# Kernel tuning notes

Hardware: AMD Instinct MI355X
Metric: run time of the kernel (lower is better)

Reference implementation:

```python
import jax, jax.numpy as jnp
import numpy as np

B, C, H, W = 16, 256, 64, 64
HID, N, SD, NH, HD, NC = 256, 300, 64, 4, 16, 80


def _conv1x1(x, w, b):
    # x: (B,Cin,H,W), w: (Cout,Cin)
    return jnp.einsum('bchw,oc->bohw', x, w) + b[None, :, None, None]


def _lin(x, w, b):
    return x @ w.T + b


def _ln(x, g, b, eps=1e-5):
    mu = x.mean(-1, keepdims=True)
    var = ((x - mu) ** 2).mean(-1, keepdims=True)
    return (x - mu) / jnp.sqrt(var + eps) * g + b


def setup_inputs() -> dict:
    key = jax.random.key(0)
    ks = jax.random.split(key, 16)
    def w(k, shape, s=0.02):
        return jax.random.normal(k, shape, jnp.float32) * s
    return {
        'x': jax.random.normal(ks[0], (B, C, H, W), jnp.float32),
        'spotlight_sources': w(ks[1], (N, SD)),
        'pos_w': w(ks[2], (HID // 2, 2)), 'pos_b': jnp.zeros((HID // 2,), jnp.float32),
        'fp_w': w(ks[3], (HID, C)), 'fp_b': jnp.zeros((HID,), jnp.float32),
        'bn_g': jnp.ones((HID,), jnp.float32), 'bn_b': jnp.zeros((HID,), jnp.float32),
        'bn_m': jnp.zeros((HID,), jnp.float32), 'bn_v': jnp.ones((HID,), jnp.float32),
        'key_w': w(ks[4], (SD, HID)), 'key_b': jnp.zeros((SD,), jnp.float32),
        'val_w': w(ks[5], (HID, HID)), 'val_b': jnp.zeros((HID,), jnp.float32),
        'ctp_w': w(ks[6], (NC, HID)), 'ctp_b': jnp.zeros((NC,), jnp.float32),
        'bb1_w': w(ks[7], (HID, HID)), 'bb1_b': jnp.zeros((HID,), jnp.float32),
        'bbln_g': jnp.ones((HID,), jnp.float32), 'bbln_b': jnp.zeros((HID,), jnp.float32),
        'bb2_w': w(ks[8], (HID // 2, HID)), 'bb2_b': jnp.zeros((HID // 2,), jnp.float32),
        'bb3_w': w(ks[9], (4, HID // 2)), 'bb3_b': jnp.zeros((4,), jnp.float32),
        'ch1_w': w(ks[10], (HID, HID)), 'ch1_b': jnp.zeros((HID,), jnp.float32),
        'chln_g': jnp.ones((HID,), jnp.float32), 'chln_b': jnp.zeros((HID,), jnp.float32),
        'ch2_w': w(ks[11], (HID // 2, HID)), 'ch2_b': jnp.zeros((HID // 2,), jnp.float32),
        'ch3_w': w(ks[12], (1, HID // 2)), 'ch3_b': jnp.zeros((1,), jnp.float32),
    }


def _forward(x, spotlight_sources, pos_w, pos_b, fp_w, fp_b, bn_g, bn_b, bn_m, bn_v,
             key_w, key_b, val_w, val_b, ctp_w, ctp_b,
             bb1_w, bb1_b, bbln_g, bbln_b, bb2_w, bb2_b, bb3_w, bb3_b,
             ch1_w, ch1_b, chln_g, chln_b, ch2_w, ch2_b, ch3_w, ch3_b):
    Bv, _, Hh, Ww = x.shape
    # position encoding: 2-channel normalized (y, x) grid, conv1x1 to HID//2
    y = jnp.linspace(-1.0, 1.0, Hh, dtype=jnp.float32)
    xc = jnp.linspace(-1.0, 1.0, Ww, dtype=jnp.float32)
    coords = jnp.stack([jnp.broadcast_to(y[:, None], (Hh, Ww)),
                        jnp.broadcast_to(xc[None, :], (Hh, Ww))], 0)[None]  # (1,2,H,W)
    # feature_proj: conv1x1 + BatchNorm(eval) + ReLU
    feats = _conv1x1(x, fp_w, fp_b)
    feats = (feats - bn_m[None, :, None, None]) / jnp.sqrt(bn_v[None, :, None, None] + 1e-5)
    feats = jax.nn.relu(feats * bn_g[None, :, None, None] + bn_b[None, :, None, None])
    pos = jnp.broadcast_to(_conv1x1(coords, pos_w, pos_b), (Bv, HID // 2, Hh, Ww))
    comb = jnp.concatenate([feats[:, :HID // 2], pos], axis=1)  # (B,HID,H,W)
    keys = _conv1x1(comb, key_w, key_b).reshape(Bv, NH, HD, Hh * Ww)   # (B,h,d,M)
    vals = _conv1x1(comb, val_w, val_b).reshape(Bv, HID, Hh * Ww)      # (B,HID,M)
    q = spotlight_sources.reshape(N, NH, HD)                            # (N,h,d)
    logits = jnp.einsum('nhd,bhdm->bhnm', q, keys) / jnp.sqrt(jnp.float32(HD))
    attn = jax.nn.softmax(logits, axis=-1).mean(axis=1)                 # (B,N,M), head-averaged
    maps = attn.reshape(Bv, N, Hh, Ww)
    sf = jnp.einsum('bnm,bcm->bnc', attn, vals)                         # (B,N,HID)
    def head(z, w1, b1, g, bb, w2, b2, w3, b3):
        z = jax.nn.relu(_ln(_lin(z, w1, b1), g, bb))
        z = jax.nn.relu(_lin(z, w2, b2))
        return _lin(z, w3, b3)
    boxes = head(sf, bb1_w, bb1_b, bbln_g, bbln_b, bb2_w, bb2_b, bb3_w, bb3_b)
    scores = jax.nn.sigmoid(head(sf, ch1_w, ch1_b, chln_g, chln_b, ch2_w, ch2_b, ch3_w, ch3_b))
    cls = _lin(sf, ctp_w, ctp_b)
    # diversity loss: mean off-diagonal cosine similarity of attention rows
    an = attn / jnp.maximum(jnp.linalg.norm(attn, axis=2, keepdims=True), 1e-12)
    sim = jnp.einsum('bnm,bkm->bnk', an, an)
    div = (sim.sum() - jnp.einsum('bnn->', sim)) / (N * (N - 1)) * 0.1
    return boxes, scores, cls, maps, div, sf


def reference(x, spotlight_sources, pos_w, pos_b, fp_w, fp_b, bn_g, bn_b, bn_m, bn_v,
              key_w, key_b, val_w, val_b, ctp_w, ctp_b,
              bb1_w, bb1_b, bbln_g, bbln_b, bb2_w, bb2_b, bb3_w, bb3_b,
              ch1_w, ch1_b, chln_g, chln_b, ch2_w, ch2_b, ch3_w, ch3_b):
    return _forward(x, spotlight_sources, pos_w, pos_b, fp_w, fp_b, bn_g, bn_b, bn_m, bn_v,
                    key_w, key_b, val_w, val_b, ctp_w, ctp_b,
                    bb1_w, bb1_b, bbln_g, bbln_b, bb2_w, bb2_b, bb3_w, bb3_b,
                    ch1_w, ch1_b, chln_g, chln_b, ch2_w, ch2_b, ch3_w, ch3_b)
```

## Files before the change

kernel.cpp:

```cpp
#include <hip/hip_runtime.h>
#include <math.h>

#define BB 16
#define CIN 256
#define MM 4096
#define HIDC 256
#define NQ 300
#define NHH 4
#define HDD 16

#define OFF_BOXES  0
#define OFF_SCORES 19200
#define OFF_CLS    24000
#define OFF_MAPS   408000
#define OFF_DIV    20068800
#define OFF_SF     20068801

#define WS_COMB16  0
#define WS_KEYS16  8388608
#define WS_ATTN16  10485760
#define WS_T32     20316160
#define WS_T16     21544960
#define WS_VALW16  22159360
#define WS_SUMS    22192128
#define WS_NORM    22211328
#define WS_ACC     22216128
#define WS_P       22216192

#define HP_SF16   (WS_P + 0)
#define HP_Z1PRE  (WS_P + 614400)
#define HP_Z1_16  (WS_P + 1843200)
#define HP_Z2BB   (WS_P + 2457600)
#define HP_Z2CH   (WS_P + 2764800)
#define HP_HW     (WS_P + 3072000)
#define WS_Q16    (WS_P + 3200000)
#define WS_XT     25426432
#define WS_COMBT  33815040
#define WS_FPW16  42203648
#define WS_KEYW16 42220032

#define HW_BB1 0
#define HW_CH1 65536
#define HW_BB2 131072
#define HW_CH2 163840
#define HW_CTP 196608

typedef short short8 __attribute__((ext_vector_type(8)));
typedef float floatx4 __attribute__((ext_vector_type(4)));

__device__ __forceinline__ unsigned short f2bf(float f){
  unsigned int u = __float_as_uint(f);
  u = (u + 0x7FFFu + ((u >> 16) & 1u)) >> 16;
  return (unsigned short)u;
}
__device__ __forceinline__ float bf1(unsigned short u){
  return __uint_as_float((unsigned int)u << 16);
}

__global__ void zero_kernel(float* p){ p[0] = 0.f; }

__global__ __launch_bounds__(256) void zero4_kernel(float4* __restrict__ p, int n4){
  int i = blockIdx.x * 256 + threadIdx.x;
  if (i < n4) p[i] = make_float4(0.f, 0.f, 0.f, 0.f);
}

__global__ __launch_bounds__(256) void cast_sum4_kernel(const float* __restrict__ part,
                                                        unsigned short* __restrict__ dst, int n4){
  int i = blockIdx.x * 256 + threadIdx.x;
  if (i < n4){
    int b = i / 19200, r = i - b * 19200;
    const float4* p0 = (const float4*)part + (size_t)(b*4 + 0) * 19200 + r;
    const float4* p1 = (const float4*)part + (size_t)(b*4 + 1) * 19200 + r;
    const float4* p2 = (const float4*)part + (size_t)(b*4 + 2) * 19200 + r;
    const float4* p3 = (const float4*)part + (size_t)(b*4 + 3) * 19200 + r;
    float4 a = *p0, bq = *p1, c = *p2, d = *p3;
    float4 v;
    v.x = a.x + bq.x + c.x + d.x;
    v.y = a.y + bq.y + c.y + d.y;
    v.z = a.z + bq.z + c.z + d.z;
    v.w = a.w + bq.w + c.w + d.w;
    ushort4 u;
    u.x = f2bf(v.x); u.y = f2bf(v.y); u.z = f2bf(v.z); u.w = f2bf(v.w);
    ((ushort4*)dst)[i] = u;
  }
}

__global__ __launch_bounds__(256) void castq_kernel(const float* __restrict__ ss,
                                                    unsigned short* __restrict__ q16){
  int i = blockIdx.x * 256 + threadIdx.x;
  if (i < 320*64)
    q16[i] = (i < NQ*64) ? f2bf(ss[i] * 0.25f) : (unsigned short)0;
}

__global__ __launch_bounds__(256) void cast_w2_kernel(const float* __restrict__ fp_w,
    const float* __restrict__ key_w,
    unsigned short* __restrict__ fpw16, unsigned short* __restrict__ keyw16){
  int i = blockIdx.x * 256 + threadIdx.x;
  if (i < 128*256) fpw16[i] = f2bf(fp_w[i]);
  if (i < 64*256)  keyw16[i] = f2bf(key_w[i]);
}

__global__ __launch_bounds__(256) void cast_heads_kernel(
    const float* __restrict__ val_w, const float* __restrict__ bb1_w,
    const float* __restrict__ ch1_w, const float* __restrict__ bb2_w,
    const float* __restrict__ ch2_w, const float* __restrict__ ctp_w,
    unsigned short* __restrict__ valw16, unsigned short* __restrict__ hw16){
  int i = blockIdx.x * 256 + threadIdx.x;
  int T = gridDim.x * 256;
  for (int j = i; j < 65536; j += T) valw16[j] = f2bf(val_w[j]);
  for (int j = i; j < 65536; j += T) hw16[HW_BB1 + j] = f2bf(bb1_w[j]);
  for (int j = i; j < 65536; j += T) hw16[HW_CH1 + j] = f2bf(ch1_w[j]);
  for (int j = i; j < 32768; j += T) hw16[HW_BB2 + j] = f2bf(bb2_w[j]);
  for (int j = i; j < 32768; j += T) hw16[HW_CH2 + j] = f2bf(ch2_w[j]);
  for (int j = i; j < 20480; j += T) hw16[HW_CTP + j] = f2bf(ctp_w[j]);
}

__global__ __launch_bounds__(256) void pos_fill_kernel(const float* __restrict__ pos_w,
                                                       const float* __restrict__ pos_b,
                                                       unsigned short* __restrict__ comb16){
  int lin = blockIdx.x * 256 + threadIdx.x;
  int m  = (lin & 1023) * 4;
  int c  = (lin >> 10) & 127;
  int b  = lin >> 17;
  int row = m >> 6, col = m & 63;
  float y  = -1.f + 2.f * (float)row / 63.f;
  float wy = pos_w[c*2], wx = pos_w[c*2+1], pb = pos_b[c];
  float base = wy * y + pb;
  ushort4 u;
  u.x = f2bf(base + wx * (-1.f + 2.f * (float)(col+0) / 63.f));
  u.y = f2bf(base + wx * (-1.f + 2.f * (float)(col+1) / 63.f));
  u.z = f2bf(base + wx * (-1.f + 2.f * (float)(col+2) / 63.f));
  u.w = f2bf(base + wx * (-1.f + 2.f * (float)(col+3) / 63.f));
  *(ushort4*)&comb16[((size_t)(b*HIDC + 128 + c))*MM + m] = u;
}

__global__ __launch_bounds__(256) void pos_fillT_kernel(const float* __restrict__ pos_w,
                                                        const float* __restrict__ pos_b,
                                                        unsigned short* __restrict__ combT){
  int lin = blockIdx.x * 256 + threadIdx.x;
  int c4 = (lin & 31) * 4;
  int m  = lin >> 5;
  int row = m >> 6, col = m & 63;
  float y = -1.f + 2.f * (float)row / 63.f;
  float x = -1.f + 2.f * (float)col / 63.f;
  ushort4 u;
  u.x = f2bf(pos_w[(c4+0)*2] * y + pos_w[(c4+0)*2+1] * x + pos_b[c4+0]);
  u.y = f2bf(pos_w[(c4+1)*2] * y + pos_w[(c4+1)*2+1] * x + pos_b[c4+1]);
  u.z = f2bf(pos_w[(c4+2)*2] * y + pos_w[(c4+2)*2+1] * x + pos_b[c4+2]);
  u.w = f2bf(pos_w[(c4+3)*2] * y + pos_w[(c4+3)*2+1] * x + pos_b[c4+3]);
  #pragma unroll
  for (int b = 0; b < BB; b++)
    *(ushort4*)&combT[((size_t)b*MM + m)*CIN + 128 + c4] = u;
}

template<bool INF32>
__global__ __launch_bounds__(256) void transpose_kernel(
    const void* __restrict__ in, unsigned short* __restrict__ outp){
  int b = blockIdx.z;
  int m0 = blockIdx.x * 64;
  int r0 = blockIdx.y * 64;
  __shared__ unsigned short lds[64][68];
  int t = threadIdx.x;
  if (INF32){
    const float* ib = (const float*)in + (size_t)b * CIN * MM;
    #pragma unroll
    for (int j = 0; j < 4; j++){
      int lin = j*256 + t;
      int rr = lin >> 4;
      int m4 = (lin & 15) * 4;
      float4 v = *(const float4*)&ib[(size_t)(r0 + rr)*MM + m0 + m4];
      lds[m4+0][rr] = f2bf(v.x);
      lds[m4+1][rr] = f2bf(v.y);
      lds[m4+2][rr] = f2bf(v.z);
      lds[m4+3][rr] = f2bf(v.w);
    }
  } else {
    const unsigned short* ib = (const unsigned short*)in + (size_t)b * CIN * MM;
    #pragma unroll
    for (int j = 0; j < 4; j++){
      int lin = j*256 + t;
      int rr = lin >> 4;
      int m4 = (lin & 15) * 4;
      ushort4 v = *(const ushort4*)&ib[(size_t)(r0 + rr)*MM + m0 + m4];
      lds[m4+0][rr] = v.x; lds[m4+1][rr] = v.y;
      lds[m4+2][rr] = v.z; lds[m4+3][rr] = v.w;
    }
  }
  __syncthreads();
  unsigned short* ob = outp + (size_t)b * MM * CIN;
  #pragma unroll
  for (int j = 0; j < 4; j++){
    int lin = j*256 + t;
    int mm = lin >> 4;
    int c4 = (lin & 15) * 4;
    ushort4 u;
    u.x = lds[mm][c4+0]; u.y = lds[mm][c4+1];
    u.z = lds[mm][c4+2]; u.w = lds[mm][c4+3];
    *(ushort4*)&ob[(size_t)(m0 + mm)*CIN + r0 + c4] = u;
  }
}

__global__ __launch_bounds__(64) void comb_mfma_kernel(
    const unsigned short* __restrict__ fpw16, const unsigned short* __restrict__ xT16,
    const float* __restrict__ fp_b, const float* __restrict__ bn_g,
    const float* __restrict__ bn_b, const float* __restrict__ bn_m,
    const float* __restrict__ bn_v, unsigned short* __restrict__ comb16){
  int b = blockIdx.z;
  const unsigned short* Bb = xT16 + (size_t)b * MM * CIN;
  unsigned short* cb = comb16 + (size_t)b * HIDC * MM;
  int lane = threadIdx.x;
  int r16 = lane & 15;
  int ko  = (lane >> 4) * 8;
  const unsigned short* arow[4];
  const unsigned short* brow[4];
  #pragma unroll
  for (int i = 0; i < 4; i++){
    arow[i] = fpw16 + (size_t)(blockIdx.y*64 + i*16 + r16) * CIN + ko;
    brow[i] = Bb + (size_t)(blockIdx.x*64 + i*16 + r16) * CIN + ko;
  }
  floatx4 acc[4][4];
  #pragma unroll
  for (int i = 0; i < 4; i++)
    #pragma unroll
    for (int j = 0; j < 4; j++)
      acc[i][j] = (floatx4){0.f, 0.f, 0.f, 0.f};
  short8 a[4], bv[4], a2[4], b2[4];
  #pragma unroll
  for (int i = 0; i < 4; i++){
    a[i]  = *(const short8*)(arow[i]);
    bv[i] = *(const short8*)(brow[i]);
  }
  for (int k = 32; k < CIN; k += 32){
    #pragma unroll
    for (int i = 0; i < 4; i++){
      a2[i] = *(const short8*)(arow[i] + k);
      b2[i] = *(const short8*)(brow[i] + k);
    }
    #pragma unroll
    for (int i = 0; i < 4; i++)
      #pragma unroll
      for (int j = 0; j < 4; j++)
        acc[i][j] = __builtin_amdgcn_mfma_f32_16x16x32_bf16(a[i], bv[j], acc[i][j], 0, 0, 0);
    #pragma unroll
    for (int i = 0; i < 4; i++){ a[i] = a2[i]; bv[i] = b2[i]; }
  }
  #pragma unroll
  for (int i = 0; i < 4; i++)
    #pragma unroll
    for (int j = 0; j < 4; j++)
      acc[i][j] = __builtin_amdgcn_mfma_f32_16x16x32_bf16(a[i], bv[j], acc[i][j], 0, 0, 0);
  int cq = lane & 15, rq = (lane >> 4) * 4;
  #pragma unroll
  for (int i = 0; i < 4; i++){
    #pragma unroll
    for (int reg = 0; reg < 4; reg++){
      int rr = blockIdx.y*64 + i*16 + rq + reg;
      float sc  = rsqrtf(bn_v[rr] + 1e-5f);
      float mul = sc * bn_g[rr];
      float ofs = (fp_b[rr] - bn_m[rr]) * mul + bn_b[rr];
      #pragma unroll
      for (int j = 0; j < 4; j++){
        int cc = blockIdx.x*64 + j*16 + cq;
        float v = fmaxf(acc[i][j][reg] * mul + ofs, 0.f);
        cb[(size_t)rr * MM + cc] = f2bf(v);
      }
    }
  }
}


__global__ __launch_bounds__(256) void attn_sums_kernel(
    const unsigned short* __restrict__ q16, const unsigned short* __restrict__ keysT,
    float* __restrict__ sums){
  int b = blockIdx.z, ny = blockIdx.y, mx = blockIdx.x;
  int tid = threadIdx.x, w = tid >> 6, lane = tid & 63;
  int n0 = ny * 64;
  int l15 = lane & 15, qh = lane >> 4;
  int ko = (qh & 1) * 8;
  bool lo = lane < 32;
  const unsigned short* kT = keysT + (size_t)b * MM * 64;
  int mwb = mx*128 + w*32;
  __shared__ unsigned short qlds[64][72];
  __shared__ float spart[4][NHH][64];
  for (int c = tid; c < 512; c += 256){
    int r = c >> 3, d8 = (c & 7) * 8;
    *(short8*)&qlds[r][d8] = *(const short8*)&q16[(size_t)(n0 + r)*64 + d8];
  }
  __syncthreads();
  short8 zz = {0,0,0,0,0,0,0,0};
  #pragma unroll 1
  for (int h = 0; h < NHH; h++){
    short8 bq[4];
    #pragma unroll
    for (int ni = 0; ni < 4; ni++)
      bq[ni] = lo ? *(const short8*)&qlds[ni*16 + l15][h*16 + ko] : zz;
    float sacc[4] = {0.f, 0.f, 0.f, 0.f};
    #pragma unroll
    for (int ms = 0; ms < 2; ms++){
      int m = mwb + ms*16 + l15;
      short8 a = lo ? *(const short8*)&kT[(size_t)m*64 + h*16 + ko] : zz;
      #pragma unroll
      for (int ni = 0; ni < 4; ni++){
        floatx4 l = __builtin_amdgcn_mfma_f32_16x16x32_bf16(a, bq[ni],
                        (floatx4){0.f,0.f,0.f,0.f}, 0, 0, 0);
        sacc[ni] += __expf(l[0]) + __expf(l[1]) + __expf(l[2]) + __expf(l[3]);
      }
    }
    #pragma unroll
    for (int ni = 0; ni < 4; ni++){
      float v = sacc[ni];
      v += __shfl_xor(v, 16); v += __shfl_xor(v, 32);
      if (lane < 16) spart[w][h][ni*16 + lane] = v;
    }
  }
  __syncthreads();
  if (tid < NHH*64){
    int h = tid >> 6, r = tid & 63, n = n0 + r;
    if (n < NQ){
      float v = spart[0][h][r] + spart[1][h][r] + spart[2][h][r] + spart[3][h][r];
      atomicAdd(&sums[((size_t)b*NHH + h)*NQ + n], v);
    }
  }
}

__global__ __launch_bounds__(256) void attn_emit_kernel(
    const unsigned short* __restrict__ q16, const unsigned short* __restrict__ keysT,
    const float* __restrict__ sums, float* __restrict__ maps,
    unsigned short* __restrict__ attn16, float* __restrict__ norms){
  int b = blockIdx.z, ny = blockIdx.y, mx = blockIdx.x;
  int tid = threadIdx.x, w = tid >> 6, lane = tid & 63;
  int n0 = ny * 64;
  int l15 = lane & 15, qh = lane >> 4;
  int ko = (qh & 1) * 8;
  bool lo = lane < 32;
  __shared__ unsigned short qlds[64][72];
  __shared__ float inv_s[NHH][64];
  __shared__ float npart[4][64];
  for (int c = tid; c < 512; c += 256){
    int r = c >> 3, d8 = (c & 7) * 8;
    *(short8*)&qlds[r][d8] = *(const short8*)&q16[(size_t)(n0 + r)*64 + d8];
  }
  if (tid < NHH*64){
    int h = tid >> 6, r = tid & 63, n = n0 + r;
    inv_s[h][r] = (n < NQ) ? 0.25f / sums[((size_t)b*NHH + h)*NQ + n] : 0.f;
  }
  __syncthreads();
  const unsigned short* kT = keysT + (size_t)b * MM * 64;
  int mwb = mx*128 + w*32;
  short8 zz = {0,0,0,0,0,0,0,0};
  float nacc[4] = {0.f, 0.f, 0.f, 0.f};
  float* mb = maps + (size_t)b * NQ * MM;
  unsigned short* ab = attn16 + (size_t)b * NQ * MM;
  #pragma unroll 1
  for (int ms = 0; ms < 2; ms++){
    asm volatile("" ::: "memory");
    int mbase = mwb + ms*16;
    int mk = mbase + l15;
    floatx4 o[4];
    #pragma unroll
    for (int ni = 0; ni < 4; ni++) o[ni] = (floatx4){0.f,0.f,0.f,0.f};
    #pragma unroll
    for (int h = 0; h < NHH; h++){
      short8 a = lo ? *(const short8*)&kT[(size_t)mk*64 + h*16 + ko] : zz;
      #pragma unroll
      for (int ni = 0; ni < 4; ni++){
        short8 bq = lo ? *(const short8*)&qlds[ni*16 + l15][h*16 + ko] : zz;
        floatx4 l = __builtin_amdgcn_mfma_f32_16x16x32_bf16(a, bq,
                        (floatx4){0.f,0.f,0.f,0.f}, 0, 0, 0);
        float iv = inv_s[h][ni*16 + l15];
        o[ni][0] += __expf(l[0]) * iv;
        o[ni][1] += __expf(l[1]) * iv;
        o[ni][2] += __expf(l[2]) * iv;
        o[ni][3] += __expf(l[3]) * iv;
      }
    }
    #pragma unroll
    for (int ni = 0; ni < 4; ni++){
      nacc[ni] += o[ni][0]*o[ni][0] + o[ni][1]*o[ni][1]
                + o[ni][2]*o[ni][2] + o[ni][3]*o[ni][3];
      int n = n0 + ni*16 + l15;
      if (n < NQ){
        size_t off = (size_t)n*MM + mbase + qh*4;
        float4 v; v.x = o[ni][0]; v.y = o[ni][1]; v.z = o[ni][2]; v.w = o[ni][3];
        *(float4*)&mb[off] = v;
        ushort4 u;
        u.x = f2bf(v.x); u.y = f2bf(v.y); u.z = f2bf(v.z); u.w = f2bf(v.w);
        *(ushort4*)&ab[off] = u;
      }
    }
  }
  #pragma unroll
  for (int ni = 0; ni < 4; ni++){
    float v = nacc[ni];
    v += __shfl_xor(v, 16); v += __shfl_xor(v, 32);
    if (lane < 16) npart[w][ni*16 + lane] = v;
  }
  __syncthreads();
  if (tid < 64){
    int n = n0 + tid;
    if (n < NQ){
      float v = npart[0][tid] + npart[1][tid] + npart[2][tid] + npart[3][tid];
      atomicAdd(&norms[(size_t)b*NQ + n], v);
    }
  }
}

template<bool RELU>
__global__ __launch_bounds__(64) void mfma_nt_kernel(
    const unsigned short* __restrict__ A, size_t sA,
    const unsigned short* __restrict__ B, size_t sB,
    const float* __restrict__ bias,
    float* __restrict__ C, unsigned short* __restrict__ C16,
    size_t sC, int ldc, int Mr, int Nc, int K){
  int bz = blockIdx.z;
  const unsigned short* Ab = A + (size_t)bz * sA;
  const unsigned short* Bb = B + (size_t)bz * sB;
  int lane = threadIdx.x;
  int r16 = lane & 15;
  int ko  = (lane >> 4) * 8;
  const unsigned short* arow[4];
  const unsigned short* brow[4];
  #pragma unroll
  for (int i = 0; i < 4; i++){
    int m = blockIdx.y*64 + i*16 + r16;
    if (m > Mr - 1) m = Mr - 1;
    arow[i] = Ab + (size_t)m * K + ko;
    int n = blockIdx.x*64 + i*16 + r16;
    if (n > Nc - 1) n = Nc - 1;
    brow[i] = Bb + (size_t)n * K + ko;
  }
  floatx4 acc[4][4];
  #pragma unroll
  for (int i = 0; i < 4; i++)
    #pragma unroll
    for (int j = 0; j < 4; j++)
      acc[i][j] = (floatx4){0.f, 0.f, 0.f, 0.f};
  short8 a[4], bv[4], a2[4], b2[4];
  #pragma unroll
  for (int i = 0; i < 4; i++){
    a[i]  = *(const short8*)(arow[i]);
    bv[i] = *(const short8*)(brow[i]);
  }
  for (int k = 32; k < K; k += 32){
    #pragma unroll
    for (int i = 0; i < 4; i++){
      a2[i] = *(const short8*)(arow[i] + k);
      b2[i] = *(const short8*)(brow[i] + k);
    }
    #pragma unroll
    for (int i = 0; i < 4; i++)
      #pragma unroll
      for (int j = 0; j < 4; j++)
        acc[i][j] = __builtin_amdgcn_mfma_f32_16x16x32_bf16(a[i], bv[j], acc[i][j], 0, 0, 0);
    #pragma unroll
    for (int i = 0; i < 4; i++){ a[i] = a2[i]; bv[i] = b2[i]; }
  }
  #pragma unroll
  for (int i = 0; i < 4; i++)
    #pragma unroll
    for (int j = 0; j < 4; j++)
      acc[i][j] = __builtin_amdgcn_mfma_f32_16x16x32_bf16(a[i], bv[j], acc[i][j], 0, 0, 0);
  int cq = lane & 15, rq = (lane >> 4) * 4;
  #pragma unroll
  for (int j = 0; j < 4; j++){
    int cc = blockIdx.x*64 + j*16 + cq;
    if (cc >= Nc) continue;
    float bv_ = bias ? bias[cc] : 0.f;
    #pragma unroll
    for (int i = 0; i < 4; i++){
      int rbase = blockIdx.y*64 + i*16 + rq;
      #pragma unroll
      for (int reg = 0; reg < 4; reg++){
        int rr = rbase + reg;
        if (rr < Mr){
          float v = acc[i][j][reg] + bv_;
          if (RELU) v = fmaxf(v, 0.f);
          size_t o = (size_t)bz * sC + (size_t)rr * ldc + cc;
          if (C)   C[o] = v;
          if (C16) C16[o] = f2bf(v);
        }
      }
    }
  }
}

__global__ __launch_bounds__(64) void mfma_nt_splitk_kernel(
    const unsigned short* __restrict__ A, size_t sA,
    const unsigned short* __restrict__ B, size_t sB,
    float* __restrict__ C, size_t sC, int ldc, int Mr, int K, int kchunk){
  int nks = K / kchunk;
  int bz = blockIdx.z / nks;
  int kz = blockIdx.z % nks;
  const unsigned short* Ab = A + (size_t)bz * sA + (size_t)kz * kchunk;
  const unsigned short* Bb = B + (size_t)bz * sB + (size_t)kz * kchunk;
  int lane = threadIdx.x;
  int r16 = lane & 15;
  int ko  = (lane >> 4) * 8;
  const unsigned short* arow[4];
  const unsigned short* brow[4];
  #pragma unroll
  for (int i = 0; i < 4; i++){
    int m = blockIdx.y*64 + i*16 + r16;
    if (m > Mr - 1) m = Mr - 1;
    arow[i] = Ab + (size_t)m * K + ko;
    int n = blockIdx.x*64 + i*16 + r16;
    brow[i] = Bb + (size_t)n * K + ko;
  }
  floatx4 acc[4][4];
  #pragma unroll
  for (int i = 0; i < 4; i++)
    #pragma unroll
    for (int j = 0; j < 4; j++)
      acc[i][j] = (floatx4){0.f, 0.f, 0.f, 0.f};
  short8 a[4], bv[4], a2[4], b2[4];
  #pragma unroll
  for (int i = 0; i < 4; i++){
    a[i]  = *(const short8*)(arow[i]);
    bv[i] = *(const short8*)(brow[i]);
  }
  for (int k = 32; k < kchunk; k += 32){
    #pragma unroll
    for (int i = 0; i < 4; i++){
      a2[i] = *(const short8*)(arow[i] + k);
      b2[i] = *(const short8*)(brow[i] + k);
    }
    #pragma unroll
    for (int i = 0; i < 4; i++)
      #pragma unroll
      for (int j = 0; j < 4; j++)
        acc[i][j] = __builtin_amdgcn_mfma_f32_16x16x32_bf16(a[i], bv[j], acc[i][j], 0, 0, 0);
    #pragma unroll
    for (int i = 0; i < 4; i++){ a[i] = a2[i]; bv[i] = b2[i]; }
  }
  #pragma unroll
  for (int i = 0; i < 4; i++)
    #pragma unroll
    for (int j = 0; j < 4; j++)
      acc[i][j] = __builtin_amdgcn_mfma_f32_16x16x32_bf16(a[i], bv[j], acc[i][j], 0, 0, 0);
  int cq = lane & 15, rq = (lane >> 4) * 4;
  #pragma unroll
  for (int j = 0; j < 4; j++){
    int cc = blockIdx.x*64 + j*16 + cq;
    #pragma unroll
    for (int i = 0; i < 4; i++){
      int rbase = blockIdx.y*64 + i*16 + rq;
      #pragma unroll
      for (int reg = 0; reg < 4; reg++){
        int rr = rbase + reg;
        if (rr < Mr)
          C[(size_t)blockIdx.z * sC + (size_t)rr * ldc + cc] = acc[i][j][reg];
      }
    }
  }
}

__global__ __launch_bounds__(256) void ln_relu_kernel(const float* __restrict__ zin,
    const float* __restrict__ g, const float* __restrict__ bvec,
    unsigned short* __restrict__ zout){
  int row = blockIdx.x * 4 + (threadIdx.x >> 6);
  int lane = threadIdx.x & 63;
  float4 v = *(const float4*)&zin[(size_t)row * 256 + lane * 4];
  float s = v.x + v.y + v.z + v.w;
  #pragma unroll
  for (int off = 32; off >= 1; off >>= 1) s += __shfl_xor(s, off);
  float mean = s * (1.f/256.f);
  float dx = v.x - mean, dy = v.y - mean, dz = v.z - mean, dw = v.w - mean;
  float sq = dx*dx + dy*dy + dz*dz + dw*dw;
  #pragma unroll
  for (int off = 32; off >= 1; off >>= 1) sq += __shfl_xor(sq, off);
  float inv = rsqrtf(sq * (1.f/256.f) + 1e-5f);
  float4 gv = *(const float4*)&g[lane * 4];
  float4 bb = *(const float4*)&bvec[lane * 4];
  ushort4 u;
  u.x = f2bf(fmaxf(dx*inv*gv.x + bb.x, 0.f));
  u.y = f2bf(fmaxf(dy*inv*gv.y + bb.y, 0.f));
  u.z = f2bf(fmaxf(dz*inv*gv.z + bb.z, 0.f));
  u.w = f2bf(fmaxf(dw*inv*gv.w + bb.w, 0.f));
  *(ushort4*)&zout[(size_t)row * 256 + lane * 4] = u;
}

__global__ __launch_bounds__(256) void head3_kernel(
    const unsigned short* __restrict__ z2bb, const unsigned short* __restrict__ z2ch,
    const float* __restrict__ bb3_w, const float* __restrict__ bb3_b,
    const float* __restrict__ ch3_w, const float* __restrict__ ch3_b,
    float* __restrict__ boxes, float* __restrict__ scores){
  int row = blockIdx.x * 4 + (threadIdx.x >> 6);
  int lane = threadIdx.x & 63;
  float zb0 = bf1(z2bb[(size_t)row*128 + 2*lane]);
  float zb1 = bf1(z2bb[(size_t)row*128 + 2*lane + 1]);
  float zc0 = bf1(z2ch[(size_t)row*128 + 2*lane]);
  float zc1 = bf1(z2ch[(size_t)row*128 + 2*lane + 1]);
  float acc[5];
  #pragma unroll
  for (int o = 0; o < 4; o++)
    acc[o] = bb3_w[o*128 + 2*lane]*zb0 + bb3_w[o*128 + 2*lane + 1]*zb1;
  acc[4] = ch3_w[2*lane]*zc0 + ch3_w[2*lane + 1]*zc1;
  #pragma unroll
  for (int o = 0; o < 5; o++){
    float v = acc[o];
    #pragma unroll
    for (int off = 32; off >= 1; off >>= 1) v += __shfl_xor(v, off);
    acc[o] = v;
  }
  if (lane == 0){
    #pragma unroll
    for (int o = 0; o < 4; o++)
      boxes[(size_t)row*4 + o] = acc[o] + bb3_b[o];
    float sv = acc[4] + ch3_b[0];
    scores[row] = 1.f / (1.f + __expf(-sv));
  }
}

__global__ __launch_bounds__(256) void simdiv_kernel(const unsigned short* __restrict__ attn16,
    const float* __restrict__ norms, float* __restrict__ acc){
  int b = blockIdx.y;
  int m = blockIdx.x * 256 + threadIdx.x;
  __shared__ float inv_s[NQ];
  __shared__ float red[4];
  for (int i = threadIdx.x; i < NQ; i += 256)
    inv_s[i] = 1.f / fmaxf(sqrtf(norms[(size_t)b * NQ + i]), 1e-12f);
  __syncthreads();
  const unsigned short* ab = attn16 + (size_t)b * NQ * MM;
  float S = 0.f;
  for (int n = 0; n < NQ; n++)
    S += bf1(ab[(size_t)n * MM + m]) * inv_s[n];
  float p = S * S;
  #pragma unroll
  for (int off = 32; off >= 1; off >>= 1) p += __shfl_xor(p, off);
  int w = threadIdx.x >> 6, lane = threadIdx.x & 63;
  if (lane == 0) red[w] = p;
  __syncthreads();
  if (threadIdx.x == 0) atomicAdd(acc, red[0] + red[1] + red[2] + red[3]);
}

__global__ void finalize_kernel(const float* __restrict__ acc, float* __restrict__ out_div){
  out_div[0] = (acc[0] - (float)(BB * NQ)) / (float)(NQ * (NQ - 1)) * 0.1f;
}

extern "C" void kernel_launch(void* const* d_in, const int* in_sizes, int n_in,
                              void* d_out, int out_size, void* d_ws, size_t ws_size,
                              hipStream_t stream){
  const float* x      = (const float*)d_in[0];
  const float* ss     = (const float*)d_in[1];
  const float* pos_w  = (const float*)d_in[2];
  const float* pos_b  = (const float*)d_in[3];
  const float* fp_w   = (const float*)d_in[4];
  const float* fp_b   = (const float*)d_in[5];
  const float* bn_g   = (const float*)d_in[6];
  const float* bn_b   = (const float*)d_in[7];
  const float* bn_m   = (const float*)d_in[8];
  const float* bn_v   = (const float*)d_in[9];
  const float* key_w  = (const float*)d_in[10];
  const float* key_b  = (const float*)d_in[11];
  const float* val_w  = (const float*)d_in[12];
  const float* val_b  = (const float*)d_in[13];
  const float* ctp_w  = (const float*)d_in[14];
  const float* ctp_b  = (const float*)d_in[15];
  const float* bb1_w  = (const float*)d_in[16];
  const float* bb1_b  = (const float*)d_in[17];
  const float* bbln_g = (const float*)d_in[18];
  const float* bbln_b = (const float*)d_in[19];
  const float* bb2_w  = (const float*)d_in[20];
  const float* bb2_b  = (const float*)d_in[21];
  const float* bb3_w  = (const float*)d_in[22];
  const float* bb3_b  = (const float*)d_in[23];
  const float* ch1_w  = (const float*)d_in[24];
  const float* ch1_b  = (const float*)d_in[25];
  const float* chln_g = (const float*)d_in[26];
  const float* chln_b = (const float*)d_in[27];
  const float* ch2_w  = (const float*)d_in[28];
  const float* ch2_b  = (const float*)d_in[29];
  const float* ch3_w  = (const float*)d_in[30];
  const float* ch3_b  = (const float*)d_in[31];

  float* out    = (float*)d_out;
  float* boxes  = out + OFF_BOXES;
  float* scores = out + OFF_SCORES;
  float* cls    = out + OFF_CLS;
  float* maps   = out + OFF_MAPS;
  float* divp   = out + OFF_DIV;
  float* sfout  = out + OFF_SF;

  float* ws = (float*)d_ws;
  unsigned short* comb16 = (unsigned short*)(ws + WS_COMB16);
  unsigned short* keysT  = (unsigned short*)(ws + WS_KEYS16);
  unsigned short* attn16 = (unsigned short*)(ws + WS_ATTN16);
  unsigned short* t16    = (unsigned short*)(ws + WS_T16);
  unsigned short* valw16 = (unsigned short*)(ws + WS_VALW16);
  float* sums  = ws + WS_SUMS;
  float* norms = ws + WS_NORM;
  float* dacc  = ws + WS_ACC;
  unsigned short* sf16   = (unsigned short*)(ws + HP_SF16);
  float*          z1pre  = ws + HP_Z1PRE;
  unsigned short* z1_16  = (unsigned short*)(ws + HP_Z1_16);
  unsigned short* z2bb16 = (unsigned short*)(ws + HP_Z2BB);
  unsigned short* z2ch16 = (unsigned short*)(ws + HP_Z2CH);
  unsigned short* hw16   = (unsigned short*)(ws + HP_HW);
  unsigned short* q16    = (unsigned short*)(ws + WS_Q16);
  unsigned short* xT16   = (unsigned short*)(ws + WS_XT);
  float*          tpart  = ws + WS_XT;
  unsigned short* combT  = (unsigned short*)(ws + WS_COMBT);
  unsigned short* fpw16  = (unsigned short*)(ws + WS_FPW16);
  unsigned short* keyw16 = (unsigned short*)(ws + WS_KEYW16);

  zero_kernel<<<1, 1, 0, stream>>>(dacc);
  zero4_kernel<<<24, 256, 0, stream>>>((float4*)sums, 6000);
  castq_kernel<<<80, 256, 0, stream>>>(ss, q16);
  cast_w2_kernel<<<128, 256, 0, stream>>>(fp_w, key_w, fpw16, keyw16);

  transpose_kernel<true><<<dim3(64,4,16), 256, 0, stream>>>(x, xT16);
  pos_fill_kernel<<<8192, 256, 0, stream>>>(pos_w, pos_b, comb16);
  pos_fillT_kernel<<<512, 256, 0, stream>>>(pos_w, pos_b, combT);
  comb_mfma_kernel<<<dim3(64,2,16), 64, 0, stream>>>(
      fpw16, xT16, fp_b, bn_g, bn_b, bn_m, bn_v, comb16);
  transpose_kernel<false><<<dim3(64,2,16), 256, 0, stream>>>(comb16, combT);
  mfma_nt_kernel<false><<<dim3(1,64,16), 64, 0, stream>>>(
      combT, (size_t)MM*CIN, keyw16, 0, key_b,
      nullptr, keysT, (size_t)MM*64, 64, MM, 64, CIN);

  attn_sums_kernel<<<dim3(32,5,16), 256, 0, stream>>>(q16, keysT, sums);
  attn_emit_kernel<<<dim3(32,5,16), 256, 0, stream>>>(q16, keysT, sums, maps, attn16, norms);

  mfma_nt_splitk_kernel<<<dim3(4,5,BB*4), 64, 0, stream>>>(
      attn16, (size_t)NQ*MM, comb16, (size_t)HIDC*MM,
      tpart, (size_t)NQ*HIDC, HIDC, NQ, MM, MM/4);
  cast_sum4_kernel<<<1200, 256, 0, stream>>>(tpart, t16, 307200);
  cast_heads_kernel<<<256, 256, 0, stream>>>(val_w, bb1_w, ch1_w, bb2_w, ch2_w, ctp_w, valw16, hw16);
  mfma_nt_kernel<false><<<dim3(4,5,BB), 64, 0, stream>>>(
      t16, (size_t)NQ*HIDC, valw16, 0, val_b,
      sfout, sf16, (size_t)NQ*HIDC, HIDC, NQ, HIDC, HIDC);

  mfma_nt_kernel<false><<<dim3(4,75,1), 64, 0, stream>>>(
      sf16, 0, hw16 + HW_BB1, 0, bb1_b, z1pre, nullptr, 0, 256, 4800, 256, 256);
  ln_relu_kernel<<<1200, 256, 0, stream>>>(z1pre, bbln_g, bbln_b, z1_16);
  mfma_nt_kernel<true><<<dim3(2,75,1), 64, 0, stream>>>(
      z1_16, 0, hw16 + HW_BB2, 0, bb2_b, nullptr, z2bb16, 0, 128, 4800, 128, 256);
  mfma_nt_kernel<false><<<dim3(4,75,1), 64, 0, stream>>>(
      sf16, 0, hw16 + HW_CH1, 0, ch1_b, z1pre, nullptr, 0, 256, 4800, 256, 256);
  ln_relu_kernel<<<1200, 256, 0, stream>>>(z1pre, chln_g, chln_b, z1_16);
  mfma_nt_kernel<true><<<dim3(2,75,1), 64, 0, stream>>>(
      z1_16, 0, hw16 + HW_CH2, 0, ch2_b, nullptr, z2ch16, 0, 128, 4800, 128, 256);
  head3_kernel<<<1200, 256, 0, stream>>>(z2bb16, z2ch16, bb3_w, bb3_b, ch3_w, ch3_b, boxes, scores);
  mfma_nt_kernel<false><<<dim3(2,75,1), 64, 0, stream>>>(
      sf16, 0, hw16 + HW_CTP, 0, ctp_b, cls, nullptr, 0, 80, 4800, 80, 256);

  simdiv_kernel<<<dim3(16,16), 256, 0, stream>>>(attn16, norms, dacc);
  finalize_kernel<<<1, 1, 0, stream>>>(dacc, divp);
}
```

Measured before the change: 514.1 us.

## Fuse small kernels, batch head GEMMs, in-block split-K reduce, drop comb transpose

Merges several setup cast kernels and the two positional-fill kernels into single launches. The comb conv epilogue now writes the transposed layout directly, so the separate bf16 transpose pass is removed. The split-K attention-value GEMM now reduces its four K-slices in shared memory within one 256-thread block and emits bf16, removing the fp32 partial buffer and the cast_sum pass. The box and score head GEMMs and their LayerNorms are batched over z with a per-batch bias stride. Together these reduce launch count and global memory traffic, at the cost of scattered 8-byte transposed stores and a four-phase serialized LDS reduction.

```diff
diff --git a/kernel.cpp b/kernel.cpp
--- a/kernel.cpp
+++ b/kernel.cpp
@@ -19,7 +19,6 @@
 #define WS_COMB16  0
 #define WS_KEYS16  8388608
 #define WS_ATTN16  10485760
-#define WS_T32     20316160
 #define WS_T16     21544960
 #define WS_VALW16  22159360
 #define WS_SUMS    22192128
@@ -28,16 +27,17 @@
 #define WS_P       22216192
 
 #define HP_SF16   (WS_P + 0)
-#define HP_Z1PRE  (WS_P + 614400)
-#define HP_Z1_16  (WS_P + 1843200)
 #define HP_Z2BB   (WS_P + 2457600)
 #define HP_Z2CH   (WS_P + 2764800)
 #define HP_HW     (WS_P + 3072000)
+#define WS_B2     (WS_P + 3180544)
 #define WS_Q16    (WS_P + 3200000)
 #define WS_XT     25426432
 #define WS_COMBT  33815040
 #define WS_FPW16  42203648
 #define WS_KEYW16 42220032
+#define WS_Z1PRE2 42228224
+#define WS_Z1B16  44685824
 
 #define HW_BB1 0
 #define HW_CH1 65536
@@ -57,54 +57,30 @@
   return __uint_as_float((unsigned int)u << 16);
 }
 
-__global__ void zero_kernel(float* p){ p[0] = 0.f; }
-
 __global__ __launch_bounds__(256) void zero4_kernel(float4* __restrict__ p, int n4){
   int i = blockIdx.x * 256 + threadIdx.x;
   if (i < n4) p[i] = make_float4(0.f, 0.f, 0.f, 0.f);
 }
 
-__global__ __launch_bounds__(256) void cast_sum4_kernel(const float* __restrict__ part,
-                                                        unsigned short* __restrict__ dst, int n4){
+__global__ __launch_bounds__(256) void init_kernel(const float* __restrict__ ss,
+    const float* __restrict__ fp_w, const float* __restrict__ key_w,
+    unsigned short* __restrict__ q16, unsigned short* __restrict__ fpw16,
+    unsigned short* __restrict__ keyw16){
   int i = blockIdx.x * 256 + threadIdx.x;
-  if (i < n4){
-    int b = i / 19200, r = i - b * 19200;
-    const float4* p0 = (const float4*)part + (size_t)(b*4 + 0) * 19200 + r;
-    const float4* p1 = (const float4*)part + (size_t)(b*4 + 1) * 19200 + r;
-    const float4* p2 = (const float4*)part + (size_t)(b*4 + 2) * 19200 + r;
-    const float4* p3 = (const float4*)part + (size_t)(b*4 + 3) * 19200 + r;
-    float4 a = *p0, bq = *p1, c = *p2, d = *p3;
-    float4 v;
-    v.x = a.x + bq.x + c.x + d.x;
-    v.y = a.y + bq.y + c.y + d.y;
-    v.z = a.z + bq.z + c.z + d.z;
-    v.w = a.w + bq.w + c.w + d.w;
-    ushort4 u;
-    u.x = f2bf(v.x); u.y = f2bf(v.y); u.z = f2bf(v.z); u.w = f2bf(v.w);
-    ((ushort4*)dst)[i] = u;
-  }
-}
-
-__global__ __launch_bounds__(256) void castq_kernel(const float* __restrict__ ss,
-                                                    unsigned short* __restrict__ q16){
-  int i = blockIdx.x * 256 + threadIdx.x;
-  if (i < 320*64)
-    q16[i] = (i < NQ*64) ? f2bf(ss[i] * 0.25f) : (unsigned short)0;
-}
-
-__global__ __launch_bounds__(256) void cast_w2_kernel(const float* __restrict__ fp_w,
-    const float* __restrict__ key_w,
-    unsigned short* __restrict__ fpw16, unsigned short* __restrict__ keyw16){
-  int i = blockIdx.x * 256 + threadIdx.x;
-  if (i < 128*256) fpw16[i] = f2bf(fp_w[i]);
-  if (i < 64*256)  keyw16[i] = f2bf(key_w[i]);
+  int T = gridDim.x * 256;
+  for (int j = i; j < 320*64; j += T)
+    q16[j] = (j < NQ*64) ? f2bf(ss[j] * 0.25f) : (unsigned short)0;
+  for (int j = i; j < 128*256; j += T) fpw16[j] = f2bf(fp_w[j]);
+  for (int j = i; j < 64*256; j += T)  keyw16[j] = f2bf(key_w[j]);
 }
 
 __global__ __launch_bounds__(256) void cast_heads_kernel(
     const float* __restrict__ val_w, const float* __restrict__ bb1_w,
     const float* __restrict__ ch1_w, const float* __restrict__ bb2_w,
     const float* __restrict__ ch2_w, const float* __restrict__ ctp_w,
-    unsigned short* __restrict__ valw16, unsigned short* __restrict__ hw16){
+    const float* __restrict__ bb2_b, const float* __restrict__ ch2_b,
+    unsigned short* __restrict__ valw16, unsigned short* __restrict__ hw16,
+    float* __restrict__ b2){
   int i = blockIdx.x * 256 + threadIdx.x;
   int T = gridDim.x * 256;
   for (int j = i; j < 65536; j += T) valw16[j] = f2bf(val_w[j]);
@@ -113,78 +89,64 @@
   for (int j = i; j < 32768; j += T) hw16[HW_BB2 + j] = f2bf(bb2_w[j]);
   for (int j = i; j < 32768; j += T) hw16[HW_CH2 + j] = f2bf(ch2_w[j]);
   for (int j = i; j < 20480; j += T) hw16[HW_CTP + j] = f2bf(ctp_w[j]);
-}
-
-__global__ __launch_bounds__(256) void pos_fill_kernel(const float* __restrict__ pos_w,
-                                                       const float* __restrict__ pos_b,
-                                                       unsigned short* __restrict__ comb16){
+  for (int j = i; j < 128; j += T){ b2[j] = bb2_b[j]; b2[128 + j] = ch2_b[j]; }
+}
+
+__global__ __launch_bounds__(256) void pos_kernel(const float* __restrict__ pos_w,
+                                                  const float* __restrict__ pos_b,
+                                                  unsigned short* __restrict__ comb16,
+                                                  unsigned short* __restrict__ combT){
   int lin = blockIdx.x * 256 + threadIdx.x;
-  int m  = (lin & 1023) * 4;
-  int c  = (lin >> 10) & 127;
-  int b  = lin >> 17;
-  int row = m >> 6, col = m & 63;
-  float y  = -1.f + 2.f * (float)row / 63.f;
-  float wy = pos_w[c*2], wx = pos_w[c*2+1], pb = pos_b[c];
-  float base = wy * y + pb;
-  ushort4 u;
-  u.x = f2bf(base + wx * (-1.f + 2.f * (float)(col+0) / 63.f));
-  u.y = f2bf(base + wx * (-1.f + 2.f * (float)(col+1) / 63.f));
-  u.z = f2bf(base + wx * (-1.f + 2.f * (float)(col+2) / 63.f));
-  u.w = f2bf(base + wx * (-1.f + 2.f * (float)(col+3) / 63.f));
-  *(ushort4*)&comb16[((size_t)(b*HIDC + 128 + c))*MM + m] = u;
-}
-
-__global__ __launch_bounds__(256) void pos_fillT_kernel(const float* __restrict__ pos_w,
-                                                        const float* __restrict__ pos_b,
-                                                        unsigned short* __restrict__ combT){
-  int lin = blockIdx.x * 256 + threadIdx.x;
-  int c4 = (lin & 31) * 4;
-  int m  = lin >> 5;
-  int row = m >> 6, col = m & 63;
-  float y = -1.f + 2.f * (float)row / 63.f;
-  float x = -1.f + 2.f * (float)col / 63.f;
-  ushort4 u;
-  u.x = f2bf(pos_w[(c4+0)*2] * y + pos_w[(c4+0)*2+1] * x + pos_b[c4+0]);
-  u.y = f2bf(pos_w[(c4+1)*2] * y + pos_w[(c4+1)*2+1] * x + pos_b[c4+1]);
-  u.z = f2bf(pos_w[(c4+2)*2] * y + pos_w[(c4+2)*2+1] * x + pos_b[c4+2]);
-  u.w = f2bf(pos_w[(c4+3)*2] * y + pos_w[(c4+3)*2+1] * x + pos_b[c4+3]);
-  #pragma unroll
-  for (int b = 0; b < BB; b++)
-    *(ushort4*)&combT[((size_t)b*MM + m)*CIN + 128 + c4] = u;
-}
-
-template<bool INF32>
-__global__ __launch_bounds__(256) void transpose_kernel(
-    const void* __restrict__ in, unsigned short* __restrict__ outp){
+  if (lin < 2097152){
+    int m  = (lin & 1023) * 4;
+    int c  = (lin >> 10) & 127;
+    int b  = lin >> 17;
+    int row = m >> 6, col = m & 63;
+    float y  = -1.f + 2.f * (float)row / 63.f;
+    float wy = pos_w[c*2], wx = pos_w[c*2+1], pb = pos_b[c];
+    float base = wy * y + pb;
+    ushort4 u;
+    u.x = f2bf(base + wx * (-1.f + 2.f * (float)(col+0) / 63.f));
+    u.y = f2bf(base + wx * (-1.f + 2.f * (float)(col+1) / 63.f));
+    u.z = f2bf(base + wx * (-1.f + 2.f * (float)(col+2) / 63.f));
+    u.w = f2bf(base + wx * (-1.f + 2.f * (float)(col+3) / 63.f));
+    *(ushort4*)&comb16[((size_t)(b*HIDC + 128 + c))*MM + m] = u;
+  } else if (lin < 2097152 + 131072){
+    int l2 = lin - 2097152;
+    int c4 = (l2 & 31) * 4;
+    int m  = l2 >> 5;
+    int row = m >> 6, col = m & 63;
+    float y = -1.f + 2.f * (float)row / 63.f;
+    float x = -1.f + 2.f * (float)col / 63.f;
+    ushort4 u;
+    u.x = f2bf(pos_w[(c4+0)*2] * y + pos_w[(c4+0)*2+1] * x + pos_b[c4+0]);
+    u.y = f2bf(pos_w[(c4+1)*2] * y + pos_w[(c4+1)*2+1] * x + pos_b[c4+1]);
+    u.z = f2bf(pos_w[(c4+2)*2] * y + pos_w[(c4+2)*2+1] * x + pos_b[c4+2]);
+    u.w = f2bf(pos_w[(c4+3)*2] * y + pos_w[(c4+3)*2+1] * x + pos_b[c4+3]);
+    #pragma unroll
+    for (int b = 0; b < BB; b++)
+      *(ushort4*)&combT[((size_t)b*MM + m)*CIN + 128 + c4] = u;
+  }
+}
+
+__global__ __launch_bounds__(256) void transpose_x_kernel(
+    const float* __restrict__ in, unsigned short* __restrict__ outp){
   int b = blockIdx.z;
   int m0 = blockIdx.x * 64;
   int r0 = blockIdx.y * 64;
   __shared__ unsigned short lds[64][68];
   int t = threadIdx.x;
-  if (INF32){
-    const float* ib = (const float*)in + (size_t)b * CIN * MM;
-    #pragma unroll
-    for (int j = 0; j < 4; j++){
-      int lin = j*256 + t;
-      int rr = lin >> 4;
-      int m4 = (lin & 15) * 4;
-      float4 v = *(const float4*)&ib[(size_t)(r0 + rr)*MM + m0 + m4];
-      lds[m4+0][rr] = f2bf(v.x);
-      lds[m4+1][rr] = f2bf(v.y);
-      lds[m4+2][rr] = f2bf(v.z);
-      lds[m4+3][rr] = f2bf(v.w);
-    }
-  } else {
-    const unsigned short* ib = (const unsigned short*)in + (size_t)b * CIN * MM;
-    #pragma unroll
-    for (int j = 0; j < 4; j++){
-      int lin = j*256 + t;
-      int rr = lin >> 4;
-      int m4 = (lin & 15) * 4;
-      ushort4 v = *(const ushort4*)&ib[(size_t)(r0 + rr)*MM + m0 + m4];
-      lds[m4+0][rr] = v.x; lds[m4+1][rr] = v.y;
-      lds[m4+2][rr] = v.z; lds[m4+3][rr] = v.w;
-    }
+  const float* ib = in + (size_t)b * CIN * MM;
+  #pragma unroll
+  for (int j = 0; j < 4; j++){
+    int lin = j*256 + t;
+    int rr = lin >> 4;
+    int m4 = (lin & 15) * 4;
+    float4 v = *(const float4*)&ib[(size_t)(r0 + rr)*MM + m0 + m4];
+    lds[m4+0][rr] = f2bf(v.x);
+    lds[m4+1][rr] = f2bf(v.y);
+    lds[m4+2][rr] = f2bf(v.z);
+    lds[m4+3][rr] = f2bf(v.w);
   }
   __syncthreads();
   unsigned short* ob = outp + (size_t)b * MM * CIN;
@@ -204,10 +166,12 @@
     const unsigned short* __restrict__ fpw16, const unsigned short* __restrict__ xT16,
     const float* __restrict__ fp_b, const float* __restrict__ bn_g,
     const float* __restrict__ bn_b, const float* __restrict__ bn_m,
-    const float* __restrict__ bn_v, unsigned short* __restrict__ comb16){
+    const float* __restrict__ bn_v, unsigned short* __restrict__ comb16,
+    unsigned short* __restrict__ combT){
   int b = blockIdx.z;
   const unsigned short* Bb = xT16 + (size_t)b * MM * CIN;
-  unsigned short* cb = comb16 + (size_t)b * HIDC * MM;
+  unsigned short* cb  = comb16 + (size_t)b * HIDC * MM;
+  unsigned short* cTb = combT + (size_t)b * MM * CIN;
   int lane = threadIdx.x;
   int r16 = lane & 15;
   int ko  = (lane >> 4) * 8;
@@ -252,18 +216,28 @@
   int cq = lane & 15, rq = (lane >> 4) * 4;
   #pragma unroll
   for (int i = 0; i < 4; i++){
+    int rbase = blockIdx.y*64 + i*16 + rq;
+    float mul[4], ofs[4];
     #pragma unroll
     for (int reg = 0; reg < 4; reg++){
-      int rr = blockIdx.y*64 + i*16 + rq + reg;
-      float sc  = rsqrtf(bn_v[rr] + 1e-5f);
-      float mul = sc * bn_g[rr];
-      float ofs = (fp_b[rr] - bn_m[rr]) * mul + bn_b[rr];
-      #pragma unroll
-      for (int j = 0; j < 4; j++){
-        int cc = blockIdx.x*64 + j*16 + cq;
-        float v = fmaxf(acc[i][j][reg] * mul + ofs, 0.f);
-        cb[(size_t)rr * MM + cc] = f2bf(v);
-      }
+      int rr = rbase + reg;
+      float sc = rsqrtf(bn_v[rr] + 1e-5f);
+      mul[reg] = sc * bn_g[rr];
+      ofs[reg] = (fp_b[rr] - bn_m[rr]) * mul[reg] + bn_b[rr];
+    }
+    #pragma unroll
+    for (int j = 0; j < 4; j++){
+      int cc = blockIdx.x*64 + j*16 + cq;
+      ushort4 u;
+      float v0 = fmaxf(acc[i][j][0] * mul[0] + ofs[0], 0.f); u.x = f2bf(v0);
+      float v1 = fmaxf(acc[i][j][1] * mul[1] + ofs[1], 0.f); u.y = f2bf(v1);
+      float v2 = fmaxf(acc[i][j][2] * mul[2] + ofs[2], 0.f); u.z = f2bf(v2);
+      float v3 = fmaxf(acc[i][j][3] * mul[3] + ofs[3], 0.f); u.w = f2bf(v3);
+      cb[(size_t)(rbase+0) * MM + cc] = u.x;
+      cb[(size_t)(rbase+1) * MM + cc] = u.y;
+      cb[(size_t)(rbase+2) * MM + cc] = u.z;
+      cb[(size_t)(rbase+3) * MM + cc] = u.w;
+      *(ushort4*)&cTb[(size_t)cc * CIN + rbase] = u;
     }
   }
 }
@@ -409,7 +383,7 @@
 __global__ __launch_bounds__(64) void mfma_nt_kernel(
     const unsigned short* __restrict__ A, size_t sA,
     const unsigned short* __restrict__ B, size_t sB,
-    const float* __restrict__ bias,
+    const float* __restrict__ bias, int bstride,
     float* __restrict__ C, unsigned short* __restrict__ C16,
     size_t sC, int ldc, int Mr, int Nc, int K){
   int bz = blockIdx.z;
@@ -465,7 +439,7 @@
   for (int j = 0; j < 4; j++){
     int cc = blockIdx.x*64 + j*16 + cq;
     if (cc >= Nc) continue;
-    float bv_ = bias ? bias[cc] : 0.f;
+    float bv_ = bias ? bias[bz*bstride + cc] : 0.f;
     #pragma unroll
     for (int i = 0; i < 4; i++){
       int rbase = blockIdx.y*64 + i*16 + rq;
@@ -484,16 +458,15 @@
   }
 }
 
-__global__ __launch_bounds__(64) void mfma_nt_splitk_kernel(
+__global__ __launch_bounds__(256) void mfma_red4_kernel(
     const unsigned short* __restrict__ A, size_t sA,
     const unsigned short* __restrict__ B, size_t sB,
-    float* __restrict__ C, size_t sC, int ldc, int Mr, int K, int kchunk){
-  int nks = K / kchunk;
-  int bz = blockIdx.z / nks;
-  int kz = blockIdx.z % nks;
-  const unsigned short* Ab = A + (size_t)bz * sA + (size_t)kz * kchunk;
-  const unsigned short* Bb = B + (size_t)bz * sB + (size_t)kz * kchunk;
-  int lane = threadIdx.x;
+    unsigned short* __restrict__ C16, size_t sC, int ldc, int Mr, int K){
+  int bz = blockIdx.z;
+  int tid = threadIdx.x, w = tid >> 6, lane = tid & 63;
+  int kchunk = K >> 2;
+  const unsigned short* Ab = A + (size_t)bz * sA + (size_t)w * kchunk;
+  const unsigned short* Bb = B + (size_t)bz * sB + (size_t)w * kchunk;
   int r16 = lane & 15;
   int ko  = (lane >> 4) * 8;
   const unsigned short* arow[4];
@@ -537,29 +510,55 @@
     #pragma unroll
     for (int j = 0; j < 4; j++)
       acc[i][j] = __builtin_amdgcn_mfma_f32_16x16x32_bf16(a[i], bv[j], acc[i][j], 0, 0, 0);
+  __shared__ float red[64][65];
   int cq = lane & 15, rq = (lane >> 4) * 4;
-  #pragma unroll
-  for (int j = 0; j < 4; j++){
-    int cc = blockIdx.x*64 + j*16 + cq;
-    #pragma unroll
-    for (int i = 0; i < 4; i++){
-      int rbase = blockIdx.y*64 + i*16 + rq;
+  #pragma unroll 1
+  for (int ph = 0; ph < 4; ph++){
+    if (w == ph){
       #pragma unroll
-      for (int reg = 0; reg < 4; reg++){
-        int rr = rbase + reg;
-        if (rr < Mr)
-          C[(size_t)blockIdx.z * sC + (size_t)rr * ldc + cc] = acc[i][j][reg];
-      }
-    }
-  }
-}
-
-__global__ __launch_bounds__(256) void ln_relu_kernel(const float* __restrict__ zin,
-    const float* __restrict__ g, const float* __restrict__ bvec,
+      for (int i = 0; i < 4; i++)
+        #pragma unroll
+        for (int reg = 0; reg < 4; reg++){
+          int r = i*16 + rq + reg;
+          #pragma unroll
+          for (int j = 0; j < 4; j++){
+            int c = j*16 + cq;
+            if (ph == 0) red[r][c] = acc[i][j][reg];
+            else         red[r][c] += acc[i][j][reg];
+          }
+        }
+    }
+    __syncthreads();
+  }
+  unsigned short* Cb = C16 + (size_t)bz * sC;
+  for (int idx = tid; idx < 1024; idx += 256){
+    int r = idx >> 4, c4 = (idx & 15) * 4;
+    int gr = blockIdx.y*64 + r;
+    if (gr < Mr){
+      ushort4 u;
+      u.x = f2bf(red[r][c4+0]); u.y = f2bf(red[r][c4+1]);
+      u.z = f2bf(red[r][c4+2]); u.w = f2bf(red[r][c4+3]);
+      *(ushort4*)&Cb[(size_t)gr * ldc + blockIdx.x*64 + c4] = u;
+    }
+  }
+}
+
+__global__ __launch_bounds__(256) void ln_relu2_kernel(const float* __restrict__ zin,
+    const float* __restrict__ bias_b, const float* __restrict__ bias_c,
+    const float* __restrict__ g_b, const float* __restrict__ be_b,
+    const float* __restrict__ g_c, const float* __restrict__ be_c,
     unsigned short* __restrict__ zout){
+  int z = blockIdx.y;
+  const float* bias = z ? bias_c : bias_b;
+  const float* g    = z ? g_c : g_b;
+  const float* be   = z ? be_c : be_b;
+  const float* zi = zin + (size_t)z * 1228800;
+  unsigned short* zo = zout + (size_t)z * 1228800;
   int row = blockIdx.x * 4 + (threadIdx.x >> 6);
   int lane = threadIdx.x & 63;
-  float4 v = *(const float4*)&zin[(size_t)row * 256 + lane * 4];
+  float4 v = *(const float4*)&zi[(size_t)row * 256 + lane * 4];
+  float4 bi = *(const float4*)&bias[lane * 4];
+  v.x += bi.x; v.y += bi.y; v.z += bi.z; v.w += bi.w;
   float s = v.x + v.y + v.z + v.w;
   #pragma unroll
   for (int off = 32; off >= 1; off >>= 1) s += __shfl_xor(s, off);
@@ -570,13 +569,13 @@
   for (int off = 32; off >= 1; off >>= 1) sq += __shfl_xor(sq, off);
   float inv = rsqrtf(sq * (1.f/256.f) + 1e-5f);
   float4 gv = *(const float4*)&g[lane * 4];
-  float4 bb = *(const float4*)&bvec[lane * 4];
+  float4 bb = *(const float4*)&be[lane * 4];
   ushort4 u;
   u.x = f2bf(fmaxf(dx*inv*gv.x + bb.x, 0.f));
   u.y = f2bf(fmaxf(dy*inv*gv.y + bb.y, 0.f));
   u.z = f2bf(fmaxf(dz*inv*gv.z + bb.z, 0.f));
   u.w = f2bf(fmaxf(dw*inv*gv.w + bb.w, 0.f));
-  *(ushort4*)&zout[(size_t)row * 256 + lane * 4] = u;
+  *(ushort4*)&zo[(size_t)row * 256 + lane * 4] = u;
 }
 
 __global__ __launch_bounds__(256) void head3_kernel(
@@ -691,58 +690,52 @@
   float* norms = ws + WS_NORM;
   float* dacc  = ws + WS_ACC;
   unsigned short* sf16   = (unsigned short*)(ws + HP_SF16);
-  float*          z1pre  = ws + HP_Z1PRE;
-  unsigned short* z1_16  = (unsigned short*)(ws + HP_Z1_16);
   unsigned short* z2bb16 = (unsigned short*)(ws + HP_Z2BB);
   unsigned short* z2ch16 = (unsigned short*)(ws + HP_Z2CH);
   unsigned short* hw16   = (unsigned short*)(ws + HP_HW);
+  float*          b2ws   = ws + WS_B2;
   unsigned short* q16    = (unsigned short*)(ws + WS_Q16);
   unsigned short* xT16   = (unsigned short*)(ws + WS_XT);
-  float*          tpart  = ws + WS_XT;
   unsigned short* combT  = (unsigned short*)(ws + WS_COMBT);
   unsigned short* fpw16  = (unsigned short*)(ws + WS_FPW16);
   unsigned short* keyw16 = (unsigned short*)(ws + WS_KEYW16);
-
-  zero_kernel<<<1, 1, 0, stream>>>(dacc);
-  zero4_kernel<<<24, 256, 0, stream>>>((float4*)sums, 6000);
-  castq_kernel<<<80, 256, 0, stream>>>(ss, q16);
-  cast_w2_kernel<<<128, 256, 0, stream>>>(fp_w, key_w, fpw16, keyw16);
-
-  transpose_kernel<true><<<dim3(64,4,16), 256, 0, stream>>>(x, xT16);
-  pos_fill_kernel<<<8192, 256, 0, stream>>>(pos_w, pos_b, comb16);
-  pos_fillT_kernel<<<512, 256, 0, stream>>>(pos_w, pos_b, combT);
+  float*          z1pre2 = ws + WS_Z1PRE2;
+  unsigned short* z1b16  = (unsigned short*)(ws + WS_Z1B16);
+
+  zero4_kernel<<<24, 256, 0, stream>>>((float4*)sums, 6002);
+  init_kernel<<<128, 256, 0, stream>>>(ss, fp_w, key_w, q16, fpw16, keyw16);
+
+  transpose_x_kernel<<<dim3(64,4,16), 256, 0, stream>>>(x, xT16);
+  pos_kernel<<<8704, 256, 0, stream>>>(pos_w, pos_b, comb16, combT);
   comb_mfma_kernel<<<dim3(64,2,16), 64, 0, stream>>>(
-      fpw16, xT16, fp_b, bn_g, bn_b, bn_m, bn_v, comb16);
-  transpose_kernel<false><<<dim3(64,2,16), 256, 0, stream>>>(comb16, combT);
+      fpw16, xT16, fp_b, bn_g, bn_b, bn_m, bn_v, comb16, combT);
   mfma_nt_kernel<false><<<dim3(1,64,16), 64, 0, stream>>>(
-      combT, (size_t)MM*CIN, keyw16, 0, key_b,
+      combT, (size_t)MM*CIN, keyw16, 0, key_b, 0,
       nullptr, keysT, (size_t)MM*64, 64, MM, 64, CIN);
 
   attn_sums_kernel<<<dim3(32,5,16), 256, 0, stream>>>(q16, keysT, sums);
   attn_emit_kernel<<<dim3(32,5,16), 256, 0, stream>>>(q16, keysT, sums, maps, attn16, norms);
 
-  mfma_nt_splitk_kernel<<<dim3(4,5,BB*4), 64, 0, stream>>>(
+  mfma_red4_kernel<<<dim3(4,5,BB), 256, 0, stream>>>(
       attn16, (size_t)NQ*MM, comb16, (size_t)HIDC*MM,
-      tpart, (size_t)NQ*HIDC, HIDC, NQ, MM, MM/4);
-  cast_sum4_kernel<<<1200, 256, 0, stream>>>(tpart, t16, 307200);
-  cast_heads_kernel<<<256, 256, 0, stream>>>(val_w, bb1_w, ch1_w, bb2_w, ch2_w, ctp_w, valw16, hw16);
+      t16, (size_t)NQ*HIDC, HIDC, NQ, MM);
+  cast_heads_kernel<<<256, 256, 0, stream>>>(val_w, bb1_w, ch1_w, bb2_w, ch2_w, ctp_w,
+                                             bb2_b, ch2_b, valw16, hw16, b2ws);
   mfma_nt_kernel<false><<<dim3(4,5,BB), 64, 0, stream>>>(
-      t16, (size_t)NQ*HIDC, valw16, 0, val_b,
+      t16, (size_t)NQ*HIDC, valw16, 0, val_b, 0,
       sfout, sf16, (size_t)NQ*HIDC, HIDC, NQ, HIDC, HIDC);
 
-  mfma_nt_kernel<false><<<dim3(4,75,1), 64, 0, stream>>>(
-      sf16, 0, hw16 + HW_BB1, 0, bb1_b, z1pre, nullptr, 0, 256, 4800, 256, 256);
-  ln_relu_kernel<<<1200, 256, 0, stream>>>(z1pre, bbln_g, bbln_b, z1_16);
-  mfma_nt_kernel<true><<<dim3(2,75,1), 64, 0, stream>>>(
-      z1_16, 0, hw16 + HW_BB2, 0, bb2_b, nullptr, z2bb16, 0, 128, 4800, 128, 256);
-  mfma_nt_kernel<false><<<dim3(4,75,1), 64, 0, stream>>>(
-      sf16, 0, hw16 + HW_CH1, 0, ch1_b, z1pre, nullptr, 0, 256, 4800, 256, 256);
-  ln_relu_kernel<<<1200, 256, 0, stream>>>(z1pre, chln_g, chln_b, z1_16);
-  mfma_nt_kernel<true><<<dim3(2,75,1), 64, 0, stream>>>(
-      z1_16, 0, hw16 + HW_CH2, 0, ch2_b, nullptr, z2ch16, 0, 128, 4800, 128, 256);
+  mfma_nt_kernel<false><<<dim3(4,75,2), 64, 0, stream>>>(
+      sf16, 0, hw16 + HW_BB1, (size_t)(HW_CH1 - HW_BB1), nullptr, 0,
+      z1pre2, nullptr, (size_t)4800*256, 256, 4800, 256, 256);
+  ln_relu2_kernel<<<dim3(1200,2), 256, 0, stream>>>(
+      z1pre2, bb1_b, ch1_b, bbln_g, bbln_b, chln_g, chln_b, z1b16);
+  mfma_nt_kernel<true><<<dim3(2,75,2), 64, 0, stream>>>(
+      z1b16, (size_t)4800*256, hw16 + HW_BB2, (size_t)(HW_CH2 - HW_BB2), b2ws, 128,
+      nullptr, z2bb16, (size_t)4800*128, 128, 4800, 128, 256);
   head3_kernel<<<1200, 256, 0, stream>>>(z2bb16, z2ch16, bb3_w, bb3_b, ch3_w, ch3_b, boxes, scores);
   mfma_nt_kernel<false><<<dim3(2,75,1), 64, 0, stream>>>(
-      sf16, 0, hw16 + HW_CTP, 0, ctp_b, cls, nullptr, 0, 80, 4800, 80, 256);
+      sf16, 0, hw16 + HW_CTP, 0, ctp_b, 0, cls, nullptr, 0, 80, 4800, 80, 256);
 
   simdiv_kernel<<<dim3(16,16), 256, 0, stream>>>(attn16, norms, dacc);
   finalize_kernel<<<1, 1, 0, stream>>>(dacc, divp);
```

Result: faster. 500.8 us (-2.6%).
